# Performance work log

Measured on AMD Instinct MI355X. Metric: run time of the kernel, lower is better.

Reference implementation:

```python
import jax, jax.numpy as jnp
import numpy as np

B = 4096          # agents
T = 16            # input_length
GH, GW = 13, 13   # grid_size
ENC = 64          # encoder_size
INP = 32          # input_embedding
DYN = 32          # dynamic_embedding
SOC = 64          # soc_embedding_size
DEC = 128         # decoder_size
K = 32            # occupied grid cells (neighbors) per agent
NNB = B * K       # total neighbors


def lrelu(x):
    return jnp.where(x >= 0, x, 0.1 * x)


def lstm_scan(x, Wih, Whh, bih, bhh, return_seq=False):
    # PyTorch LSTM gate order: i, f, g, o. x: [T, N, in]
    N = x.shape[1]
    H = Whh.shape[1]
    xg = jnp.einsum('tni,gi->tng', x, Wih) + bih + bhh  # precompute input part

    def step(carry, g_in):
        h, c = carry
        g = g_in + h @ Whh.T
        i, f, gg, o = jnp.split(g, 4, axis=-1)
        c = jax.nn.sigmoid(f) * c + jax.nn.sigmoid(i) * jnp.tanh(gg)
        h = jax.nn.sigmoid(o) * jnp.tanh(c)
        return (h, c), (h if return_seq else None)

    h0 = jnp.zeros((N, H), x.dtype)
    (h, _), hs = jax.lax.scan(step, (h0, h0), xg)
    return hs if return_seq else h


def setup_inputs() -> dict:
    key = jax.random.key(0)
    ks = jax.random.split(key, 16)

    def lin(k, o, i):
        k1, k2 = jax.random.split(k)
        s = 1.0 / np.sqrt(i)
        return (jax.random.uniform(k1, (o, i), minval=-s, maxval=s),
                jax.random.uniform(k2, (o,), minval=-s, maxval=s))

    W_inp, b_inp = lin(ks[0], INP, 2)
    W_dym, b_dym = lin(ks[1], DYN, ENC)
    W_sp, b_sp = lin(ks[2], SOC, GH * GW * ENC)
    W_out, b_out = lin(ks[3], 5, DEC)
    Wih, bih = lin(ks[4], 4 * ENC, INP)
    Whh, bhh = lin(ks[5], 4 * ENC, ENC)
    dWih, dbih = lin(ks[6], 4 * DEC, SOC + DYN)
    dWhh, dbhh = lin(ks[7], 4 * DEC, DEC)

    hist_batch = jax.random.normal(ks[8], (T, B, 2), dtype=jnp.float32)
    nbrs_batch = jax.random.normal(ks[9], (T, NNB, 2), dtype=jnp.float32)

    # mask: exactly K occupied grid cells per agent; each occupied cell is True
    # across all ENC channels so masked_scatter_ places exactly one neighbor
    # hidden vector per occupied cell (True count == NNB * ENC).
    rng = np.random.default_rng(0)
    idx = np.argsort(rng.random((B, GH * GW)), axis=1)[:, :K]
    cells = np.zeros((B, GH * GW), dtype=bool)
    np.put_along_axis(cells, idx, True, axis=1)
    mask_batch = jnp.asarray(
        np.broadcast_to(cells.reshape(B, GH, GW, 1), (B, GH, GW, ENC)))

    return dict(hist_batch=hist_batch, nbrs_batch=nbrs_batch,
                W_inp=W_inp, b_inp=b_inp, Wih=Wih, Whh=Whh, bih=bih, bhh=bhh,
                W_dym=W_dym, b_dym=b_dym, W_sp=W_sp, b_sp=b_sp,
                dWih=dWih, dWhh=dWhh, dbih=dbih, dbhh=dbhh,
                W_out=W_out, b_out=b_out, mask_batch=mask_batch)


def reference(hist_batch, nbrs_batch, W_inp, b_inp, Wih, Whh, bih, bhh,
              W_dym, b_dym, W_sp, b_sp, dWih, dWhh, dbih, dbhh,
              W_out, b_out, mask_batch):
    # history encoder
    hist_h = lstm_scan(lrelu(hist_batch @ W_inp.T + b_inp), Wih, Whh, bih, bhh)  # [B,ENC]
    hist_enc = lrelu(hist_h @ W_dym.T + b_dym)                                   # [B,DYN]

    # neighbor encoder (shared LSTM)
    nbrs_h = lstm_scan(lrelu(nbrs_batch @ W_inp.T + b_inp), Wih, Whh, bih, bhh)  # [NNB,ENC]

    # masked_scatter_: fill True positions (row-major order) with nbrs_h values
    mflat = mask_batch.reshape(-1)
    src = nbrs_h.reshape(-1)
    pos = jnp.cumsum(mflat) - 1
    soc = jnp.where(mflat, src[jnp.clip(pos, 0, src.shape[0] - 1)],
                    jnp.zeros((), src.dtype))
    soc = soc.reshape(mask_batch.shape)                 # [B,GH,GW,ENC]
    soc = soc.transpose(0, 3, 2, 1)                     # permute(0,3,2,1)
    soc = soc.reshape(soc.shape[0], -1)                 # [B, ENC*GW*GH]
    social = lrelu(soc @ W_sp.T + b_sp)                 # [B,SOC]

    enc = jnp.concatenate([hist_enc, social], axis=1)   # [B, DYN+SOC]
    enc_seq = jnp.broadcast_to(enc, (T,) + enc.shape)   # repeat(T,1,1)
    dec = lstm_scan(enc_seq, dWih, dWhh, dbih, dbhh, return_seq=True)  # [T,B,DEC]
    out = dec.transpose(1, 0, 2) @ W_out.T + b_out      # [B,T,5]

    # outputActivation: mu_x, mu_y, exp(sig_x), exp(sig_y), tanh(rho)
    muX, muY, sX, sY, rho = jnp.split(out, 5, axis=2)
    return jnp.concatenate(
        [muX, muY, jnp.exp(sX), jnp.exp(sY), jnp.tanh(rho)], axis=2)
```

## Files before the change

kernel.cpp:

```cpp
#include <hip/hip_runtime.h>
#include <hip/hip_bf16.h>

typedef _Float16 half8 __attribute__((ext_vector_type(8)));
typedef float f32x4 __attribute__((ext_vector_type(4)));

constexpr float L2E   = 1.44269504088896340736f;
constexpr float SC_LO = 4096.0f;
constexpr float IV_LO = 1.0f / 4096.0f;

#define MFMA16(a,b,c) __builtin_amdgcn_mfma_f32_16x16x32_f16((a),(b),(c),0,0,0)

__device__ __forceinline__ float fexp2(float x){ float r; asm("v_exp_f32 %0, %1":"=v"(r):"v"(x)); return r; }
__device__ __forceinline__ float frcp(float x){ float r; asm("v_rcp_f32 %0, %1":"=v"(r):"v"(x)); return r; }

__device__ __forceinline__ float sigm_s(float y){ return frcp(1.0f + fexp2(-y)); }
__device__ __forceinline__ float tanh_s(float y){ return 1.0f - 2.0f*frcp(fexp2(y) + 1.0f); }

__global__ __launch_bounds__(256, 2)
void lstm_enc_kernel(const float* __restrict__ xh,
                     const float* __restrict__ xn,
                     const float* __restrict__ W_inp,
                     const float* __restrict__ b_inp,
                     const float* __restrict__ Wih,
                     const float* __restrict__ Whh,
                     const float* __restrict__ bih,
                     const float* __restrict__ bhh,
                     float* __restrict__ outh,
                     float* __restrict__ outn)
{
    __shared__ _Float16 h_hi[2][64*72];
    __shared__ _Float16 h_ls[2][64*72];
    const int tid = threadIdx.x;
    const int w   = tid >> 6;
    const int l   = tid & 63;
    const int l15 = l & 15, lhi = l >> 4;

    const int bid = blockIdx.x;
    const bool is_hist = (bid < 64);
    const float* x = is_hist ? xh : xn;
    float* out     = is_hist ? outh : outn;
    const int N    = is_hist ? 4096 : 131072;
    const int rbase = (is_hist ? bid : (bid - 64)) * 64;

    half8 whhH[4][2], whhLs[4][2];
    half8 wihH[4], wihLs[4];
    float bias[4];
#pragma unroll
    for (int g = 0; g < 4; ++g) {
        const int col = 16*(w + 4*g) + l15;
        const float sc = (g == 2) ? 2.0f*L2E : L2E;
#pragma unroll
        for (int kh = 0; kh < 2; ++kh)
#pragma unroll
            for (int j = 0; j < 8; ++j) {
                const float v = Whh[col*64 + kh*32 + lhi*8 + j] * sc;
                const _Float16 hi = (_Float16)v;
                whhH[g][kh][j]  = hi;
                whhLs[g][kh][j] = (_Float16)((v - (float)hi) * SC_LO);
            }
#pragma unroll
        for (int j = 0; j < 8; ++j) {
            const float v = Wih[col*32 + lhi*8 + j] * sc;
            const _Float16 hi = (_Float16)v;
            wihH[g][j]  = hi;
            wihLs[g][j] = (_Float16)((v - (float)hi) * SC_LO);
        }
        bias[g] = (bih[col] + bhh[col]) * sc;
    }
    float w0[8], w1[8], bb[8];
#pragma unroll
    for (int j = 0; j < 8; ++j) {
        const int k = lhi*8 + j;
        w0[j] = W_inp[k*2 + 0]; w1[j] = W_inp[k*2 + 1]; bb[j] = b_inp[k];
    }

    float c[4][4];
#pragma unroll
    for (int m = 0; m < 4; ++m)
#pragma unroll
        for (int j = 0; j < 4; ++j) c[m][j] = 0.0f;

    const float2* xp = (const float2*)x;
    float2 xc[4];
#pragma unroll
    for (int m = 0; m < 4; ++m)
        xc[m] = xp[(size_t)0*N + rbase + 16*m + l15];

    for (int t = 0; t < 16; ++t) {
        const int rdb = (t + 1) & 1;
        const int wrb = t & 1;
        float hnew[4][4];
#pragma unroll
        for (int m = 0; m < 4; ++m) {
            half8 eh, els;
#pragma unroll
            for (int j = 0; j < 8; ++j) {
                float v = xc[m].x * w0[j] + xc[m].y * w1[j] + bb[j];
                v = fmaxf(v, 0.1f * v);
                const _Float16 hi = (_Float16)v;
                eh[j]  = hi;
                els[j] = (_Float16)((v - (float)hi) * SC_LO);
            }
            f32x4 a0[4], a2[4];
#pragma unroll
            for (int g = 0; g < 4; ++g) {
                a0[g] = (f32x4){bias[g], bias[g], bias[g], bias[g]};
                a2[g] = (f32x4){0.f, 0.f, 0.f, 0.f};
            }
#pragma unroll
            for (int g = 0; g < 4; ++g) {
                a0[g] = MFMA16(eh,  wihH[g],  a0[g]);
                a2[g] = MFMA16(eh,  wihLs[g], a2[g]);
                a2[g] = MFMA16(els, wihH[g],  a2[g]);
            }
            if (t > 0) {
#pragma unroll
                for (int kh = 0; kh < 2; ++kh) {
                    const int off = (16*m + l15)*72 + kh*32 + lhi*8;
                    half8 ah = *(const half8*)&h_hi[rdb][off];
                    half8 as = *(const half8*)&h_ls[rdb][off];
#pragma unroll
                    for (int g = 0; g < 4; ++g) {
                        a0[g] = MFMA16(ah, whhH[g][kh],  a0[g]);
                        a2[g] = MFMA16(ah, whhLs[g][kh], a2[g]);
                        a2[g] = MFMA16(as, whhH[g][kh],  a2[g]);
                    }
                }
            }
#pragma unroll
            for (int j = 0; j < 4; ++j) {
                const float pi = a0[0][j] + a2[0][j]*IV_LO;
                const float pf = a0[1][j] + a2[1][j]*IV_LO;
                const float pg = a0[2][j] + a2[2][j]*IV_LO;
                const float po = a0[3][j] + a2[3][j]*IV_LO;
                const float si = sigm_s(pi);
                const float sf = sigm_s(pf);
                const float tg = tanh_s(pg);
                const float so = sigm_s(po);
                const float cc = sf * c[m][j] + si * tg;
                c[m][j] = cc;
                hnew[m][j] = so * tanh_s(2.0f*L2E*cc);
            }
        }
#pragma unroll
        for (int m = 0; m < 4; ++m)
#pragma unroll
            for (int j = 0; j < 4; ++j) {
                const int idx = (16*m + lhi*4 + j)*72 + 16*w + l15;
                const float v = hnew[m][j];
                const _Float16 hi = (_Float16)v;
                h_hi[wrb][idx] = hi;
                h_ls[wrb][idx] = (_Float16)((v - (float)hi) * SC_LO);
            }
        __syncthreads();
        if (t < 15) {
#pragma unroll
            for (int m = 0; m < 4; ++m)
                xc[m] = xp[(size_t)(t+1)*N + rbase + 16*m + l15];
        }
    }
    {
        const int row = tid >> 2, c0 = (tid & 3) * 16;
        const size_t g = (size_t)(rbase + row) * 64 + c0;
#pragma unroll
        for (int i = 0; i < 16; ++i) {
            const int idx = row*72 + c0 + i;
            out[g + i] = (float)h_hi[1][idx] + (float)h_ls[1][idx] * IV_LO;
        }
    }
}

__global__ __launch_bounds__(256)
void hist_enc32_kernel(const float* __restrict__ hh,
                       const float* __restrict__ W_dym,
                       const float* __restrict__ b_dym,
                       float* __restrict__ enc)
{
    const int idx = blockIdx.x * 256 + threadIdx.x;
    if (idx >= 4096 * 32) return;
    const int b = idx >> 5, s = idx & 31;
    float a = b_dym[s];
    const float* hr = hh + (size_t)b * 64;
    const float* wr = W_dym + (size_t)s * 64;
#pragma unroll
    for (int e = 0; e < 64; ++e) a += hr[e] * wr[e];
    enc[(size_t)b * 96 + s] = fmaxf(a, 0.1f * a);
}

__global__ void wsp_prep32_kernel(const float* __restrict__ W_sp,
                                  float* __restrict__ WspT)
{
    const int idx = blockIdx.x * 256 + threadIdx.x;
    if (idx >= 64 * 10816) return;
    const int s = idx / 10816, cidx = idx % 10816;
    const int e = cidx / 169, p = cidx % 169;
    WspT[((size_t)p * 64 + e) * 64 + s] = W_sp[idx];
}

__global__ void pos_prep_kernel(const void* __restrict__ mask_raw,
                                unsigned char* __restrict__ pos)
{
    const int agent = (int)((blockIdx.x * 256 + threadIdx.x) >> 6);
    const int l = threadIdx.x & 63;
    if (agent >= 4096) return;
    if (l < 32) pos[agent*32 + l] = 0;

    const unsigned char* raw = (const unsigned char*)mask_raw;
    const int* mi = (const int*)mask_raw;

    int mism = 0;
#pragma unroll
    for (int ch = 0; ch < 3; ++ch) {
        const int cc = ch*64 + l;
        if (cc < 169) {
            const unsigned char b0 = raw[cc*64], b1 = raw[cc*64 + 1];
            mism |= (b0 != 0 && b1 == 0) ? 1 : 0;
        }
    }
    const bool is_i32 = (__ballot(mism != 0) != 0ull);

    int base = 0;
#pragma unroll
    for (int ch = 0; ch < 3; ++ch) {
        const int cc = ch*64 + l;
        bool occ = false;
        if (cc < 169) {
            const size_t ei = (size_t)agent * 10816 + (size_t)cc * 64;
            occ = is_i32 ? (mi[ei] != 0) : (raw[ei] != 0);
        }
        const unsigned long long bal = __ballot(occ);
        if (occ) {
            const int rank = base + __popcll(bal & ((1ull << l) - 1ull));
            const int gh = cc / 13, gw = cc % 13;
            if (rank < 32)
                pos[agent*32 + rank] = (unsigned char)(gw*13 + gh);
        }
        base += __popcll(bal);
    }
}

__global__ __launch_bounds__(256)
void social32_kernel(const float* __restrict__ nh,
                     const float* __restrict__ WspT,
                     const float* __restrict__ b_sp,
                     const unsigned char* __restrict__ pos,
                     float* __restrict__ enc)
{
    __shared__ float part[4][64];
    __shared__ unsigned char pl[32];
    const int tid = threadIdx.x, b = blockIdx.x;
    if (tid < 32) {
        const int p = pos[b*32 + tid];
        pl[tid] = (unsigned char)(p > 168 ? 0 : p);
    }
    __syncthreads();
    const int s = tid & 63, kq = tid >> 6;
    float a = 0.f;
    for (int kk = 0; kk < 8; ++kk) {
        const int k = kq*8 + kk;
        const float* nr = nh + ((size_t)b*32 + k) * 64;
        const float* wp = WspT + (size_t)pl[k] * 4096 + s;
#pragma unroll
        for (int e = 0; e < 64; ++e) a += nr[e] * wp[(size_t)e * 64];
    }
    part[kq][s] = a;
    __syncthreads();
    if (tid < 64) {
        const float v = part[0][tid] + part[1][tid] + part[2][tid] + part[3][tid] + b_sp[tid];
        enc[(size_t)b * 96 + 32 + tid] = fmaxf(v, 0.1f * v);
    }
}

__global__ __launch_bounds__(512, 1)
void decoder_kernel(const float* __restrict__ enc,
                    const float* __restrict__ dWih,
                    const float* __restrict__ dWhh,
                    const float* __restrict__ dbih,
                    const float* __restrict__ dbhh,
                    const float* __restrict__ W_out,
                    const float* __restrict__ b_out,
                    float* __restrict__ outp)
{
    __shared__ float enc_lds[16*100];
    __shared__ _Float16 hh_t[16*136];
    __shared__ _Float16 hl_t[16*136];
    __shared__ float wout[5*132];
    __shared__ float bout[5];
    __shared__ float part[16][5][4];
    const int tid = threadIdx.x;
    const int w = tid >> 6, l = tid & 63, l15 = l & 15, lhi = l >> 4;
    const int rb = blockIdx.x * 16;

    if (tid < 384) {
        const int row = tid / 24, ch = tid % 24;
        *(float4*)&enc_lds[row*100 + ch*4] = *(const float4*)&enc[(size_t)(rb + row)*96 + ch*4];
    }
    for (int i = tid; i < 640; i += 512) { const int j = i / 128, e = i % 128; wout[j*132 + e] = W_out[i]; }
    if (tid < 5) bout[tid] = b_out[tid];
    __syncthreads();

    half8 whhH[4][4], whhLs[4][4];
    f32x4 xg0[4], xg2[4];
#pragma unroll
    for (int g = 0; g < 4; ++g) {
        const int col = 16*(8*g + w) + l15;
        const float sc = (g == 2) ? 2.0f*L2E : L2E;
#pragma unroll
        for (int kh = 0; kh < 4; ++kh)
#pragma unroll
            for (int j = 0; j < 8; ++j) {
                const float v = dWhh[col*128 + kh*32 + lhi*8 + j] * sc;
                const _Float16 hi = (_Float16)v;
                whhH[g][kh][j]  = hi;
                whhLs[g][kh][j] = (_Float16)((v - (float)hi) * SC_LO);
            }
        const float bv = (dbih[col] + dbhh[col]) * sc;
        xg0[g] = (f32x4){bv, bv, bv, bv};
        xg2[g] = (f32x4){0.f, 0.f, 0.f, 0.f};
    }
#pragma unroll
    for (int kh = 0; kh < 3; ++kh) {
        half8 eh, els;
#pragma unroll
        for (int j = 0; j < 8; ++j) {
            const float v = enc_lds[l15*100 + kh*32 + lhi*8 + j];
            const _Float16 hi = (_Float16)v;
            eh[j]  = hi;
            els[j] = (_Float16)((v - (float)hi) * SC_LO);
        }
#pragma unroll
        for (int g = 0; g < 4; ++g) {
            const int col = 16*(8*g + w) + l15;
            const float sc = (g == 2) ? 2.0f*L2E : L2E;
            half8 bH, bLs;
#pragma unroll
            for (int j = 0; j < 8; ++j) {
                const float v = dWih[col*96 + kh*32 + lhi*8 + j] * sc;
                const _Float16 hi = (_Float16)v;
                bH[j]  = hi;
                bLs[j] = (_Float16)((v - (float)hi) * SC_LO);
            }
            xg0[g] = MFMA16(eh,  bH,  xg0[g]);
            xg2[g] = MFMA16(eh,  bLs, xg2[g]);
            xg2[g] = MFMA16(els, bH,  xg2[g]);
        }
    }
    f32x4 xg[4];
#pragma unroll
    for (int g = 0; g < 4; ++g)
#pragma unroll
        for (int j = 0; j < 4; ++j) xg[g][j] = xg0[g][j] + xg2[g][j]*IV_LO;

    float c[4] = {0.f, 0.f, 0.f, 0.f};
    for (int t = 0; t < 16; ++t) {
        f32x4 a0[4], a2[4];
#pragma unroll
        for (int g = 0; g < 4; ++g) { a0[g] = xg[g]; a2[g] = (f32x4){0.f,0.f,0.f,0.f}; }
        if (t > 0) {
#pragma unroll
            for (int kh = 0; kh < 4; ++kh) {
                const int off = l15*136 + kh*32 + lhi*8;
                half8 ah = *(const half8*)&hh_t[off];
                half8 as = *(const half8*)&hl_t[off];
#pragma unroll
                for (int g = 0; g < 4; ++g) {
                    a0[g] = MFMA16(ah, whhH[g][kh],  a0[g]);
                    a2[g] = MFMA16(ah, whhLs[g][kh], a2[g]);
                    a2[g] = MFMA16(as, whhH[g][kh],  a2[g]);
                }
            }
        }
        float hnew[4];
#pragma unroll
        for (int j = 0; j < 4; ++j) {
            const float pi = a0[0][j] + a2[0][j]*IV_LO;
            const float pf = a0[1][j] + a2[1][j]*IV_LO;
            const float pg = a0[2][j] + a2[2][j]*IV_LO;
            const float po = a0[3][j] + a2[3][j]*IV_LO;
            const float si = sigm_s(pi);
            const float sf = sigm_s(pf);
            const float tg = tanh_s(pg);
            const float so = sigm_s(po);
            const float cc = sf * c[j] + si * tg;
            c[j] = cc;
            hnew[j] = so * tanh_s(2.0f*L2E*cc);
        }
        __syncthreads();
#pragma unroll
        for (int j = 0; j < 4; ++j) {
            const int idx = (lhi*4 + j)*136 + 16*w + l15;
            const float v = hnew[j];
            const _Float16 hi = (_Float16)v;
            hh_t[idx] = hi;
            hl_t[idx] = (_Float16)((v - (float)hi) * SC_LO);
        }
        __syncthreads();
        if (tid < 320) {
            const int row = tid / 20, rem = tid % 20, j5 = rem / 4, q = rem % 4;
            float pacc = 0.0f;
#pragma unroll
            for (int e = 0; e < 32; ++e) {
                const int idx = row*136 + q*32 + e;
                pacc += ((float)hh_t[idx] + (float)hl_t[idx]*IV_LO) * wout[j5*132 + q*32 + e];
            }
            part[row][j5][q] = pacc;
        }
        __syncthreads();
        if (tid < 80) {
            const int row = tid / 5, j5 = tid % 5;
            float v = part[row][j5][0] + part[row][j5][1] + part[row][j5][2] + part[row][j5][3] + bout[j5];
            if (j5 == 2 || j5 == 3) v = fexp2(v * L2E);
            else if (j5 == 4)       v = tanh_s(2.0f*L2E*v);
            outp[((size_t)(rb + row)*16 + t)*5 + j5] = v;
        }
    }
}

extern "C" void kernel_launch(void* const* d_in, const int* in_sizes, int n_in,
                              void* d_out, int out_size, void* d_ws, size_t ws_size,
                              hipStream_t stream) {
    const float* hist  = (const float*)d_in[0];
    const float* nbrs  = (const float*)d_in[1];
    const float* W_inp = (const float*)d_in[2];
    const float* b_inp = (const float*)d_in[3];
    const float* Wih   = (const float*)d_in[4];
    const float* Whh   = (const float*)d_in[5];
    const float* bih   = (const float*)d_in[6];
    const float* bhh   = (const float*)d_in[7];
    const float* W_dym = (const float*)d_in[8];
    const float* b_dym = (const float*)d_in[9];
    const float* W_sp  = (const float*)d_in[10];
    const float* b_sp  = (const float*)d_in[11];
    const float* dWih  = (const float*)d_in[12];
    const float* dWhh  = (const float*)d_in[13];
    const float* dbih  = (const float*)d_in[14];
    const float* dbhh  = (const float*)d_in[15];
    const float* W_out = (const float*)d_in[16];
    const float* b_out = (const float*)d_in[17];
    const void* mask   = (const void*)d_in[18];

    char* ws = (char*)d_ws;
    float* nh32        = (float*)(ws);
    float* hh32        = (float*)(ws + 33554432);
    float* WspT32      = (float*)(ws + 34603008);
    unsigned char* pos = (unsigned char*)(ws + 37371904);
    float* enc32       = (float*)(ws + 37502976);

    wsp_prep32_kernel<<<2704, 256, 0, stream>>>(W_sp, WspT32);
    pos_prep_kernel<<<1024, 256, 0, stream>>>(mask, pos);
    lstm_enc_kernel<<<2112, 256, 0, stream>>>(hist, nbrs, W_inp, b_inp, Wih, Whh, bih, bhh,
                                              hh32, nh32);
    hist_enc32_kernel<<<512, 256, 0, stream>>>(hh32, W_dym, b_dym, enc32);
    social32_kernel<<<4096, 256, 0, stream>>>(nh32, WspT32, b_sp, pos, enc32);
    decoder_kernel<<<256, 512, 0, stream>>>(enc32, dWih, dWhh, dbih, dbhh, W_out, b_out,
                                            (float*)d_out);
}
```

Measured before the change: 574.9 us.

## Fuse prep kernels into encoder launch, fp16 social weights, merge hist projection

Folds the W_sp transpose and the mask-to-position prep into extra blocks of the LSTM encoder launch, and folds the history dynamic projection into the social kernel. This cuts the launch count from six to three. The transposed W_sp is now stored as fp16, halving the weight traffic in the social gather at some cost in precision. It also forces the time loops in the encoder and decoder to stay rolled, likely to lower register pressure or code size.

```diff
diff --git a/kernel.cpp b/kernel.cpp
--- a/kernel.cpp
+++ b/kernel.cpp
@@ -17,7 +17,7 @@
 __device__ __forceinline__ float tanh_s(float y){ return 1.0f - 2.0f*frcp(fexp2(y) + 1.0f); }
 
 __global__ __launch_bounds__(256, 2)
-void lstm_enc_kernel(const float* __restrict__ xh,
+void mega_enc_kernel(const float* __restrict__ xh,
                      const float* __restrict__ xn,
                      const float* __restrict__ W_inp,
                      const float* __restrict__ b_inp,
@@ -25,17 +25,70 @@
                      const float* __restrict__ Whh,
                      const float* __restrict__ bih,
                      const float* __restrict__ bhh,
+                     const float* __restrict__ W_sp,
+                     const void*  __restrict__ mask_raw,
                      float* __restrict__ outh,
-                     float* __restrict__ outn)
+                     float* __restrict__ outn,
+                     _Float16* __restrict__ WspT,
+                     unsigned char* __restrict__ pos)
 {
     __shared__ _Float16 h_hi[2][64*72];
     __shared__ _Float16 h_ls[2][64*72];
     const int tid = threadIdx.x;
+    const int bid = blockIdx.x;
+
+    if (bid >= 2112) {
+        if (bid < 2112 + 2704) {
+            const int idx = (bid - 2112) * 256 + tid;
+            if (idx < 64 * 10816) {
+                const int s = idx / 10816, cidx = idx % 10816;
+                const int e = cidx / 169, p = cidx % 169;
+                WspT[((size_t)p*64 + e)*64 + s] = (_Float16)W_sp[idx];
+            }
+        } else {
+            const int agent = (bid - 4816) * 4 + (tid >> 6);
+            const int l = tid & 63;
+            if (agent < 4096) {
+                if (l < 32) pos[agent*32 + l] = 0;
+                const unsigned char* raw = (const unsigned char*)mask_raw;
+                const int* mi = (const int*)mask_raw;
+                int mism = 0;
+#pragma unroll
+                for (int ch = 0; ch < 3; ++ch) {
+                    const int cc = ch*64 + l;
+                    if (cc < 169) {
+                        const unsigned char b0 = raw[cc*64], b1 = raw[cc*64 + 1];
+                        mism |= (b0 != 0 && b1 == 0) ? 1 : 0;
+                    }
+                }
+                const bool is_i32 = (__ballot(mism != 0) != 0ull);
+                int base = 0;
+#pragma unroll
+                for (int ch = 0; ch < 3; ++ch) {
+                    const int cc = ch*64 + l;
+                    bool occ = false;
+                    if (cc < 169) {
+                        const size_t ei = (size_t)agent * 10816 + (size_t)cc * 64;
+                        occ = is_i32 ? (mi[ei] != 0) : (raw[ei] != 0);
+                    }
+                    const unsigned long long bal = __ballot(occ);
+                    if (occ) {
+                        const int rank = base + __popcll(bal & ((1ull << l) - 1ull));
+                        const int gh = cc / 13, gw = cc % 13;
+                        if (rank < 32)
+                            pos[agent*32 + rank] = (unsigned char)(gw*13 + gh);
+                    }
+                    base += __popcll(bal);
+                }
+            }
+        }
+        return;
+    }
+
     const int w   = tid >> 6;
     const int l   = tid & 63;
     const int l15 = l & 15, lhi = l >> 4;
 
-    const int bid = blockIdx.x;
     const bool is_hist = (bid < 64);
     const float* x = is_hist ? xh : xn;
     float* out     = is_hist ? outh : outn;
@@ -86,6 +139,7 @@
     for (int m = 0; m < 4; ++m)
         xc[m] = xp[(size_t)0*N + rbase + 16*m + l15];
 
+#pragma unroll 1
     for (int t = 0; t < 16; ++t) {
         const int rdb = (t + 1) & 1;
         const int wrb = t & 1;
@@ -171,80 +225,14 @@
 }
 
 __global__ __launch_bounds__(256)
-void hist_enc32_kernel(const float* __restrict__ hh,
-                       const float* __restrict__ W_dym,
-                       const float* __restrict__ b_dym,
-                       float* __restrict__ enc)
-{
-    const int idx = blockIdx.x * 256 + threadIdx.x;
-    if (idx >= 4096 * 32) return;
-    const int b = idx >> 5, s = idx & 31;
-    float a = b_dym[s];
-    const float* hr = hh + (size_t)b * 64;
-    const float* wr = W_dym + (size_t)s * 64;
-#pragma unroll
-    for (int e = 0; e < 64; ++e) a += hr[e] * wr[e];
-    enc[(size_t)b * 96 + s] = fmaxf(a, 0.1f * a);
-}
-
-__global__ void wsp_prep32_kernel(const float* __restrict__ W_sp,
-                                  float* __restrict__ WspT)
-{
-    const int idx = blockIdx.x * 256 + threadIdx.x;
-    if (idx >= 64 * 10816) return;
-    const int s = idx / 10816, cidx = idx % 10816;
-    const int e = cidx / 169, p = cidx % 169;
-    WspT[((size_t)p * 64 + e) * 64 + s] = W_sp[idx];
-}
-
-__global__ void pos_prep_kernel(const void* __restrict__ mask_raw,
-                                unsigned char* __restrict__ pos)
-{
-    const int agent = (int)((blockIdx.x * 256 + threadIdx.x) >> 6);
-    const int l = threadIdx.x & 63;
-    if (agent >= 4096) return;
-    if (l < 32) pos[agent*32 + l] = 0;
-
-    const unsigned char* raw = (const unsigned char*)mask_raw;
-    const int* mi = (const int*)mask_raw;
-
-    int mism = 0;
-#pragma unroll
-    for (int ch = 0; ch < 3; ++ch) {
-        const int cc = ch*64 + l;
-        if (cc < 169) {
-            const unsigned char b0 = raw[cc*64], b1 = raw[cc*64 + 1];
-            mism |= (b0 != 0 && b1 == 0) ? 1 : 0;
-        }
-    }
-    const bool is_i32 = (__ballot(mism != 0) != 0ull);
-
-    int base = 0;
-#pragma unroll
-    for (int ch = 0; ch < 3; ++ch) {
-        const int cc = ch*64 + l;
-        bool occ = false;
-        if (cc < 169) {
-            const size_t ei = (size_t)agent * 10816 + (size_t)cc * 64;
-            occ = is_i32 ? (mi[ei] != 0) : (raw[ei] != 0);
-        }
-        const unsigned long long bal = __ballot(occ);
-        if (occ) {
-            const int rank = base + __popcll(bal & ((1ull << l) - 1ull));
-            const int gh = cc / 13, gw = cc % 13;
-            if (rank < 32)
-                pos[agent*32 + rank] = (unsigned char)(gw*13 + gh);
-        }
-        base += __popcll(bal);
-    }
-}
-
-__global__ __launch_bounds__(256)
-void social32_kernel(const float* __restrict__ nh,
-                     const float* __restrict__ WspT,
-                     const float* __restrict__ b_sp,
-                     const unsigned char* __restrict__ pos,
-                     float* __restrict__ enc)
+void social_kernel(const float* __restrict__ nh,
+                   const float* __restrict__ hh,
+                   const _Float16* __restrict__ WspT,
+                   const float* __restrict__ b_sp,
+                   const float* __restrict__ W_dym,
+                   const float* __restrict__ b_dym,
+                   const unsigned char* __restrict__ pos,
+                   float* __restrict__ enc)
 {
     __shared__ float part[4][64];
     __shared__ unsigned char pl[32];
@@ -259,15 +247,23 @@
     for (int kk = 0; kk < 8; ++kk) {
         const int k = kq*8 + kk;
         const float* nr = nh + ((size_t)b*32 + k) * 64;
-        const float* wp = WspT + (size_t)pl[k] * 4096 + s;
-#pragma unroll
-        for (int e = 0; e < 64; ++e) a += nr[e] * wp[(size_t)e * 64];
+        const _Float16* wp = WspT + (size_t)pl[k] * 4096 + s;
+#pragma unroll
+        for (int e = 0; e < 64; ++e) a += nr[e] * (float)wp[(size_t)e * 64];
     }
     part[kq][s] = a;
     __syncthreads();
     if (tid < 64) {
         const float v = part[0][tid] + part[1][tid] + part[2][tid] + part[3][tid] + b_sp[tid];
         enc[(size_t)b * 96 + 32 + tid] = fmaxf(v, 0.1f * v);
+    } else if (tid >= 64 && tid < 96) {
+        const int so = tid - 64;
+        float ah = b_dym[so];
+        const float* hr = hh + (size_t)b * 64;
+        const float* wr = W_dym + (size_t)so * 64;
+#pragma unroll
+        for (int e = 0; e < 64; ++e) ah += hr[e] * wr[e];
+        enc[(size_t)b * 96 + so] = fmaxf(ah, 0.1f * ah);
     }
 }
 
@@ -352,6 +348,7 @@
         for (int j = 0; j < 4; ++j) xg[g][j] = xg0[g][j] + xg2[g][j]*IV_LO;
 
     float c[4] = {0.f, 0.f, 0.f, 0.f};
+#pragma unroll 1
     for (int t = 0; t < 16; ++t) {
         f32x4 a0[4], a2[4];
 #pragma unroll
@@ -442,16 +439,13 @@
     char* ws = (char*)d_ws;
     float* nh32        = (float*)(ws);
     float* hh32        = (float*)(ws + 33554432);
-    float* WspT32      = (float*)(ws + 34603008);
-    unsigned char* pos = (unsigned char*)(ws + 37371904);
-    float* enc32       = (float*)(ws + 37502976);
-
-    wsp_prep32_kernel<<<2704, 256, 0, stream>>>(W_sp, WspT32);
-    pos_prep_kernel<<<1024, 256, 0, stream>>>(mask, pos);
-    lstm_enc_kernel<<<2112, 256, 0, stream>>>(hist, nbrs, W_inp, b_inp, Wih, Whh, bih, bhh,
-                                              hh32, nh32);
-    hist_enc32_kernel<<<512, 256, 0, stream>>>(hh32, W_dym, b_dym, enc32);
-    social32_kernel<<<4096, 256, 0, stream>>>(nh32, WspT32, b_sp, pos, enc32);
+    _Float16* WspT16   = (_Float16*)(ws + 34603008);
+    unsigned char* pos = (unsigned char*)(ws + 35987456);
+    float* enc32       = (float*)(ws + 36118528);
+
+    mega_enc_kernel<<<5840, 256, 0, stream>>>(hist, nbrs, W_inp, b_inp, Wih, Whh, bih, bhh,
+                                              W_sp, mask, hh32, nh32, WspT16, pos);
+    social_kernel<<<4096, 256, 0, stream>>>(nh32, hh32, WspT16, b_sp, W_dym, b_dym, pos, enc32);
     decoder_kernel<<<256, 512, 0, stream>>>(enc32, dWih, dWhh, dbih, dbhh, W_out, b_out,
                                             (float*)d_out);
 }
```

Measured after the change: 547.1 us. 4.8% less time.
